# Kernel tuning notes

Measured on AMD Instinct MI355X. Metric: run time of the kernel, lower is better.

Reference implementation:

```python
import jax, jax.numpy as jnp
import numpy as np

U = 3072; I = 3072; N = U + I
D = 128; H = 4; HD = D // H
K = 10; BLOCKS = 2; RAW = 1280; DFF = 4 * D


def _pe_table(n, d):
    # standard sinusoidal positional encoding table [n, d]
    pos = jnp.arange(n, dtype=jnp.float32)[:, None]
    div = jnp.exp(jnp.arange(0, d, 2, dtype=jnp.float32) * (-np.log(10000.0) / d))
    ang = pos * div[None, :]
    pe = jnp.zeros((n, d), jnp.float32)
    return pe.at[:, 0::2].set(jnp.sin(ang)).at[:, 1::2].set(jnp.cos(ang))


def _ln(x, g, b, eps=1e-5):
    m = jnp.mean(x, -1, keepdims=True)
    v = jnp.var(x, -1, keepdims=True)
    return (x - m) * jax.lax.rsqrt(v + eps) * g + b


def _encoder(x, aw, ab, w1, b1, w2, b2, lng, lnb):
    # post-LN transformer encoder layer over sequence of all nodes of one type
    S = x.shape[0]
    q = (x @ aw[0] + ab[0]).reshape(S, H, HD)
    k = (x @ aw[1] + ab[1]).reshape(S, H, HD)
    v = (x @ aw[2] + ab[2]).reshape(S, H, HD)
    attn = jax.nn.softmax(jnp.einsum('shd,thd->hst', q, k) / np.sqrt(HD), axis=-1)
    o = jnp.einsum('hst,thd->shd', attn, v).reshape(S, D) @ aw[3] + ab[3]
    x = _ln(x + o, lng[0], lnb[0])
    f = jax.nn.relu(x @ w1 + b1) @ w2 + b2
    return _ln(x + f, lng[1], lnb[1])


def _topk_adj(emb, adj):
    # AttentionSampling(alpha=0.5, top_k=K): blend embedding similarity with adj,
    # keep adjacency entries at the per-row top-K positions (no_grad in original).
    e = jax.lax.stop_gradient(emb)
    score = 0.5 * (e @ e.T) + 0.5 * jax.lax.stop_gradient(adj)
    _, idx = jax.lax.top_k(score, K)  # [N, K]
    mask = jnp.zeros(adj.shape, adj.dtype).at[jnp.arange(adj.shape[0])[:, None], idx].set(1.0)
    return jax.lax.stop_gradient(mask) * adj


def _forward(adj, raw_nodes, proj_w, proj_b, user_emb, item_emb, visual_sim,
             alpha, pe_gate_w, pe_gate_b,
             u_attn_w, u_attn_b, u_ffn_w1, u_ffn_b1, u_ffn_w2, u_ffn_b2, u_ln_g, u_ln_b,
             i_attn_w, i_attn_b, i_ffn_w1, i_ffn_b1, i_ffn_w2, i_ffn_b2, i_ln_g, i_ln_b):
    eps = 1e-7
    # symmetric normalization of the item visual similarity matrix
    deg = jnp.sum(visual_sim, axis=1)
    dinv = jnp.power(deg + eps, -0.5)
    sim_norm = dinv[:, None] * visual_sim * dinv[None, :]
    pe = _pe_table(N, D)

    raw = raw_nodes @ proj_w + proj_b                       # [N, D]
    learned = jnp.concatenate([user_emb, item_emb], axis=0)  # [N, D]
    x = alpha * raw + (1.0 - alpha) * learned

    embeds_list = [x]
    for _ in range(BLOCKS):
        prev = embeds_list[-1]
        adj_topk = _topk_adj(prev, adj)
        # gnn_message_passing: spmm + visual similarity propagation on items
        cur = adj_topk @ prev
        cur = cur.at[U:].add(alpha * (sim_norm @ prev[U:]))
        # gated positional encoding on sampled nodes (all rows have top-K edges)
        gate = jax.nn.sigmoid(cur @ pe_gate_w + pe_gate_b)
        cur = cur + gate * pe
        u = _encoder(cur[:U], u_attn_w, u_attn_b, u_ffn_w1, u_ffn_b1,
                     u_ffn_w2, u_ffn_b2, u_ln_g, u_ln_b)
        it = _encoder(cur[U:], i_attn_w, i_attn_b, i_ffn_w1, i_ffn_b1,
                      i_ffn_w2, i_ffn_b2, i_ln_g, i_ln_b)
        embeds_list.append(jnp.concatenate([u, it], axis=0))

    w = jnp.linspace(1.0, 0.5, len(embeds_list))
    final = sum(wi * e for wi, e in zip(list(w), embeds_list))
    return final


def setup_inputs() -> dict:
    key = jax.random.key(0)
    ks = jax.random.split(key, 24)
    s = lambda i, shape, sc=0.05: jax.random.normal(ks[i], shape, jnp.float32) * sc
    u = jax.random.uniform(ks[20], (N, N), jnp.float32)
    adj = jnp.where(u < 0.005, 1.0, 0.0).astype(jnp.float32)  # sparse-pattern adjacency
    vs = jax.random.uniform(ks[21], (I, I), jnp.float32)
    visual_sim = (vs + vs.T) * 0.5
    return dict(
        adj=adj,
        raw_nodes=s(0, (N, RAW), 1.0),
        proj_w=s(1, (RAW, D)), proj_b=jnp.zeros((D,), jnp.float32),
        user_emb=s(2, (U, D), 0.1), item_emb=s(3, (I, D), 0.1),
        visual_sim=visual_sim,
        alpha=jnp.float32(0.5),
        pe_gate_w=s(4, (D, D), 0.01), pe_gate_b=jnp.full((D,), 0.5, jnp.float32),
        u_attn_w=s(5, (4, D, D)), u_attn_b=jnp.zeros((4, D), jnp.float32),
        u_ffn_w1=s(6, (D, DFF)), u_ffn_b1=jnp.zeros((DFF,), jnp.float32),
        u_ffn_w2=s(7, (DFF, D)), u_ffn_b2=jnp.zeros((D,), jnp.float32),
        u_ln_g=jnp.ones((2, D), jnp.float32), u_ln_b=jnp.zeros((2, D), jnp.float32),
        i_attn_w=s(8, (4, D, D)), i_attn_b=jnp.zeros((4, D), jnp.float32),
        i_ffn_w1=s(9, (D, DFF)), i_ffn_b1=jnp.zeros((DFF,), jnp.float32),
        i_ffn_w2=s(10, (DFF, D)), i_ffn_b2=jnp.zeros((D,), jnp.float32),
        i_ln_g=jnp.ones((2, D), jnp.float32), i_ln_b=jnp.zeros((2, D), jnp.float32),
    )


def reference(adj, raw_nodes, proj_w, proj_b, user_emb, item_emb, visual_sim, alpha,
              pe_gate_w, pe_gate_b,
              u_attn_w, u_attn_b, u_ffn_w1, u_ffn_b1, u_ffn_w2, u_ffn_b2, u_ln_g, u_ln_b,
              i_attn_w, i_attn_b, i_ffn_w1, i_ffn_b1, i_ffn_w2, i_ffn_b2, i_ln_g, i_ln_b):
    final = _forward(adj, raw_nodes, proj_w, proj_b, user_emb, item_emb, visual_sim,
                     alpha, pe_gate_w, pe_gate_b,
                     u_attn_w, u_attn_b, u_ffn_w1, u_ffn_b1, u_ffn_w2, u_ffn_b2, u_ln_g, u_ln_b,
                     i_attn_w, i_attn_b, i_ffn_w1, i_ffn_b1, i_ffn_w2, i_ffn_b2, i_ln_g, i_ln_b)
    return final, final[:U], final[U:]
```

## Files before the change

### kernel.cpp

```cpp
#include <hip/hip_runtime.h>
#include <math.h>

#define NTOT 6144
#define UU   3072
#define II   3072
#define DD   128
#define SS   3072
#define DFF2 512
#define HH   4

__global__ void pe_k(float* __restrict__ pe) {
  int idx = blockIdx.x * 256 + threadIdx.x;
  if (idx >= NTOT * 64) return;
  int pos = idx >> 6, j = idx & 63;
  float ex = (2.0f * (float)j) * (-0.07195578415606394f);
  float dv = expf(ex);
  float ang = (float)pos * dv;
  pe[(size_t)pos * DD + 2 * j]     = sinf(ang);
  pe[(size_t)pos * DD + 2 * j + 1] = cosf(ang);
}

__global__ void dinv_k(const float* __restrict__ vs, float* __restrict__ dinv) {
  int i = blockIdx.x, tid = threadIdx.x;
  __shared__ float red[256];
  float s = 0.f;
  const float* row = vs + (size_t)i * II;
  for (int j = tid; j < II; j += 256) s += row[j];
  red[tid] = s; __syncthreads();
  for (int st = 128; st > 0; st >>= 1) { if (tid < st) red[tid] += red[tid + st]; __syncthreads(); }
  if (tid == 0) dinv[i] = 1.0f / sqrtf(red[0] + 1e-7f);
}

__device__ __forceinline__ void gemm_core(
    const float* __restrict__ A, const float* __restrict__ B,
    int N, int K, int bm, int bn, int k0beg, int k0end,
    float (*As)[68], float (*Bs)[68], float (&acc)[4][4]) {
  const int tid = threadIdx.x;
  const int am = tid >> 2, ak = (tid & 3) * 4;
  const int bk = tid >> 4, bnc = (tid & 15) * 4;
  const float* Ap = A + (size_t)(bm + am) * K + ak;
  const float* Bp = B + (size_t)bk * N + bn + bnc;
  float4 av = *(const float4*)(Ap + k0beg);
  float4 bv = *(const float4*)(Bp + (size_t)k0beg * N);
  const int tx = tid & 15, ty = tid >> 4;
  for (int k0 = k0beg; k0 < k0end; k0 += 16) {
    __syncthreads();
    As[ak + 0][am] = av.x; As[ak + 1][am] = av.y;
    As[ak + 2][am] = av.z; As[ak + 3][am] = av.w;
    *(float4*)&Bs[bk][bnc] = bv;
    __syncthreads();
    if (k0 + 16 < k0end) {
      av = *(const float4*)(Ap + k0 + 16);
      bv = *(const float4*)(Bp + (size_t)(k0 + 16) * N);
    }
#pragma unroll
    for (int kq = 0; kq < 16; ++kq) {
      float4 a4 = *(const float4*)&As[kq][ty * 4];
      float4 b4 = *(const float4*)&Bs[kq][tx * 4];
      const float* ap = (const float*)&a4;
      const float* bp = (const float*)&b4;
#pragma unroll
      for (int i = 0; i < 4; ++i)
#pragma unroll
        for (int j = 0; j < 4; ++j)
          acc[i][j] = fmaf(ap[i], bp[j], acc[i][j]);
    }
  }
}

template<bool RELU>
__global__ __launch_bounds__(256, 4) void gemm_k(
    const float* __restrict__ A, const float* __restrict__ B,
    const float* __restrict__ bias, float* __restrict__ C,
    int M, int N, int K) {
  __shared__ float As[16][68];
  __shared__ float Bs[16][68];
  const int bm = blockIdx.y * 64, bn = blockIdx.x * 64;
  float acc[4][4] = {{0.f}};
  gemm_core(A, B, N, K, bm, bn, 0, K, As, Bs, acc);
  const int tx = threadIdx.x & 15, ty = threadIdx.x >> 4;
#pragma unroll
  for (int i = 0; i < 4; ++i) {
    int row = bm + ty * 4 + i;
    float4 o; float* op = (float*)&o;
#pragma unroll
    for (int j = 0; j < 4; ++j) {
      float v = acc[i][j] + (bias ? bias[bn + tx * 4 + j] : 0.0f);
      if (RELU) v = fmaxf(v, 0.0f);
      op[j] = v;
    }
    *(float4*)&C[(size_t)row * N + bn + tx * 4] = o;
  }
}

template<bool RELU>
__global__ __launch_bounds__(256, 4) void gemm2_k(
    const float* __restrict__ A, const float* __restrict__ Bu,
    const float* __restrict__ Bi, const float* __restrict__ biasu,
    const float* __restrict__ biasi, float* __restrict__ C,
    int N, int K) {
  __shared__ float As[16][68];
  __shared__ float Bs[16][68];
  const int bm = blockIdx.y * 64, bn = blockIdx.x * 64;
  const float* B    = (bm < UU) ? Bu : Bi;
  const float* bias = (bm < UU) ? biasu : biasi;
  float acc[4][4] = {{0.f}};
  gemm_core(A, B, N, K, bm, bn, 0, K, As, Bs, acc);
  const int tx = threadIdx.x & 15, ty = threadIdx.x >> 4;
#pragma unroll
  for (int i = 0; i < 4; ++i) {
    int row = bm + ty * 4 + i;
    float4 o; float* op = (float*)&o;
#pragma unroll
    for (int j = 0; j < 4; ++j) {
      float v = acc[i][j] + bias[bn + tx * 4 + j];
      if (RELU) v = fmaxf(v, 0.0f);
      op[j] = v;
    }
    *(float4*)&C[(size_t)row * N + bn + tx * 4] = o;
  }
}

__global__ __launch_bounds__(256, 4) void gemm_qkv2_k(
    const float* __restrict__ A, const float* __restrict__ Wu,
    const float* __restrict__ Wi, const float* __restrict__ Bu,
    const float* __restrict__ Bi, float* __restrict__ Cb) {
  __shared__ float As[16][68];
  __shared__ float Bs[16][68];
  const int mat = blockIdx.x >> 1;
  const int bn = (blockIdx.x & 1) * 64;
  const int bm = blockIdx.y * 64;
  const float* W    = ((bm < UU) ? Wu : Wi) + (size_t)mat * DD * DD;
  const float* bias = ((bm < UU) ? Bu : Bi) + mat * DD;
  float* C = Cb + (size_t)mat * NTOT * DD;
  float acc[4][4] = {{0.f}};
  gemm_core(A, W, DD, DD, bm, bn, 0, DD, As, Bs, acc);
  const int tx = threadIdx.x & 15, ty = threadIdx.x >> 4;
#pragma unroll
  for (int i = 0; i < 4; ++i) {
    int row = bm + ty * 4 + i;
    float4 o; float* op = (float*)&o;
#pragma unroll
    for (int j = 0; j < 4; ++j) op[j] = acc[i][j] + bias[bn + tx * 4 + j];
    *(float4*)&C[(size_t)row * DD + bn + tx * 4] = o;
  }
}

__global__ __launch_bounds__(256, 4) void gemm_blend_k(
    const float* __restrict__ A, const float* __restrict__ B,
    const float* __restrict__ bias, const float* __restrict__ ue,
    const float* __restrict__ ie, const float* __restrict__ alpha_p,
    float* __restrict__ C, int K) {
  __shared__ float As[16][68];
  __shared__ float Bs[16][68];
  const int bm = blockIdx.y * 64, bn = blockIdx.x * 64;
  float acc[4][4] = {{0.f}};
  gemm_core(A, B, DD, K, bm, bn, 0, K, As, Bs, acc);
  const int tx = threadIdx.x & 15, ty = threadIdx.x >> 4;
  float a = alpha_p[0];
#pragma unroll
  for (int i = 0; i < 4; ++i) {
    int row = bm + ty * 4 + i;
    const float* lrn = (row < UU) ? &ue[(size_t)row * DD]
                                  : &ie[(size_t)(row - UU) * DD];
    float4 lv = *(const float4*)&lrn[bn + tx * 4];
    const float* lp = (const float*)&lv;
    float4 o; float* op = (float*)&o;
#pragma unroll
    for (int j = 0; j < 4; ++j)
      op[j] = a * (acc[i][j] + bias[bn + tx * 4 + j]) + (1.0f - a) * lp[j];
    *(float4*)&C[(size_t)row * DD + bn + tx * 4] = o;
  }
}

__global__ __launch_bounds__(256, 4) void gemm_gate_k(
    const float* __restrict__ Acur, const float* __restrict__ B,
    const float* __restrict__ bias, const float* __restrict__ pe,
    float* __restrict__ Cout) {
  __shared__ float As[16][68];
  __shared__ float Bs[16][68];
  const int bm = blockIdx.y * 64, bn = blockIdx.x * 64;
  float acc[4][4] = {{0.f}};
  gemm_core(Acur, B, DD, DD, bm, bn, 0, DD, As, Bs, acc);
  const int tx = threadIdx.x & 15, ty = threadIdx.x >> 4;
#pragma unroll
  for (int i = 0; i < 4; ++i) {
    int row = bm + ty * 4 + i;
    float4 cv = *(const float4*)&Acur[(size_t)row * DD + bn + tx * 4];
    float4 pv = *(const float4*)&pe[(size_t)row * DD + bn + tx * 4];
    const float* cp = (const float*)&cv;
    const float* pp = (const float*)&pv;
    float4 o; float* op = (float*)&o;
#pragma unroll
    for (int j = 0; j < 4; ++j) {
      float v = acc[i][j] + bias[bn + tx * 4 + j];
      float g = 1.0f / (1.0f + expf(-v));
      op[j] = cp[j] + g * pp[j];
    }
    *(float4*)&Cout[(size_t)row * DD + bn + tx * 4] = o;
  }
}

__global__ __launch_bounds__(256, 4) void gemm_sk_k(
    const float* __restrict__ A, const float* __restrict__ B,
    const float* __restrict__ dinv, const float* __restrict__ alpha_p,
    float* __restrict__ C, int KCH) {
  __shared__ float As[16][68];
  __shared__ float Bs[16][68];
  const int N = DD, K = II;
  const int tid = threadIdx.x;
  const int am = tid >> 2, ak = (tid & 3) * 4;
  const int bk = tid >> 4, bnc = (tid & 15) * 4;
  const int bm = blockIdx.y * 64, bn = blockIdx.x * 64;
  const int kb = blockIdx.z * KCH, ke = kb + KCH;
  const float* Ap = A + (size_t)(bm + am) * K + ak;
  const float* Bp = B + (size_t)bk * N + bn + bnc;
  float4 av = *(const float4*)(Ap + kb);
  float4 bv = *(const float4*)(Bp + (size_t)kb * N);
  const int tx = tid & 15, ty = tid >> 4;
  float acc[4][4] = {{0.f}};
  for (int k0 = kb; k0 < ke; k0 += 16) {
    float ds = dinv[k0 + bk];
    __syncthreads();
    As[ak + 0][am] = av.x; As[ak + 1][am] = av.y;
    As[ak + 2][am] = av.z; As[ak + 3][am] = av.w;
    float4 sb = bv;
    sb.x *= ds; sb.y *= ds; sb.z *= ds; sb.w *= ds;
    *(float4*)&Bs[bk][bnc] = sb;
    __syncthreads();
    if (k0 + 16 < ke) {
      av = *(const float4*)(Ap + k0 + 16);
      bv = *(const float4*)(Bp + (size_t)(k0 + 16) * N);
    }
#pragma unroll
    for (int kq = 0; kq < 16; ++kq) {
      float4 a4 = *(const float4*)&As[kq][ty * 4];
      float4 b4 = *(const float4*)&Bs[kq][tx * 4];
      const float* ap = (const float*)&a4;
      const float* bp = (const float*)&b4;
#pragma unroll
      for (int i = 0; i < 4; ++i)
#pragma unroll
        for (int j = 0; j < 4; ++j)
          acc[i][j] = fmaf(ap[i], bp[j], acc[i][j]);
    }
  }
  float sc = alpha_p[0];
#pragma unroll
  for (int i = 0; i < 4; ++i) {
    int row = bm + ty * 4 + i;
    float rs = dinv[row] * sc;
#pragma unroll
    for (int j = 0; j < 4; ++j)
      atomicAdd(&C[(size_t)row * N + bn + tx * 4 + j], acc[i][j] * rs);
  }
}

__device__ __forceinline__ void ins10(float (&v)[10], int (&ix)[10], float cv, int ci) {
  if (!((cv > v[9]) || (cv == v[9] && ci < ix[9]))) return;
#pragma unroll
  for (int q = 0; q < 10; ++q) {
    bool b = (cv > v[q]) || (cv == v[q] && ci < ix[q]);
    float ov = v[q]; int oi = ix[q];
    if (b) { v[q] = cv; ix[q] = ci; cv = ov; ci = oi; }
  }
}

__global__ __launch_bounds__(256, 3) void topk_part_k(
    const float* __restrict__ E, const float* __restrict__ adj,
    float* __restrict__ topv, int* __restrict__ topi) {
  const int quarter = blockIdx.x;
  const int i0 = blockIdx.y * 32;
  const int jb = quarter * 1536;
  const int tid = threadIdx.x;
  const int a0 = tid & 15;
  const int b0 = tid >> 4;

  __shared__ __align__(16) unsigned char sm[50688];
  float4* Ei4 = (float4*)sm;
  float4* Ej4 = (float4*)(sm + 16896);
  float* dv   = (float*)(sm + 0);
  int*   di   = (int*)  (sm + 20736);
  float* redv = (float*)(sm + 41472);
  int*   redi = (int*)  (sm + 43648);
  float* wlv  = (float*)(sm + 45824);
  int*   wli  = (int*)  (sm + 47104);

  for (int p = 0; p < 4; ++p) {
    int l = tid + p * 256, r = l >> 5, c = l & 31;
    Ei4[r * 33 + c] = ((const float4*)(E + (size_t)(i0 + r) * DD))[c];
  }

  float v0[10], v1[10]; int y0[10], y1[10];
#pragma unroll
  for (int q = 0; q < 10; ++q) { v0[q] = -INFINITY; v1[q] = -INFINITY; y0[q] = 0x7fffffff; y1[q] = 0x7fffffff; }

  const float* arow0 = adj + (size_t)(i0 + a0) * NTOT;
  const float* arow1 = adj + (size_t)(i0 + a0 + 16) * NTOT;

  for (int jt = 0; jt < 24; ++jt) {
    const int jc = jb + jt * 64;
    __syncthreads();
#pragma unroll
    for (int p = 0; p < 8; ++p) {
      int l = tid + p * 256, r = l >> 5, c = l & 31;
      Ej4[r * 33 + c] = ((const float4*)(E + (size_t)(jc + r) * DD))[c];
    }
    __syncthreads();
    float ad0[4], ad1[4];
#pragma unroll
    for (int u = 0; u < 4; ++u) {
      int jg = jc + b0 + 16 * u;
      ad0[u] = arow0[jg];
      ad1[u] = arow1[jg];
    }
    float d0[4] = {0.f, 0.f, 0.f, 0.f}, d1[4] = {0.f, 0.f, 0.f, 0.f};
#pragma unroll 8
    for (int kq = 0; kq < 32; ++kq) {
      float4 aa = Ei4[a0 * 33 + kq];
      float4 ab = Ei4[(a0 + 16) * 33 + kq];
#pragma unroll
      for (int u = 0; u < 4; ++u) {
        float4 b = Ej4[(b0 + 16 * u) * 33 + kq];
        d0[u] = fmaf(aa.x, b.x, fmaf(aa.y, b.y, fmaf(aa.z, b.z, fmaf(aa.w, b.w, d0[u]))));
        d1[u] = fmaf(ab.x, b.x, fmaf(ab.y, b.y, fmaf(ab.z, b.z, fmaf(ab.w, b.w, d1[u]))));
      }
    }
#pragma unroll
    for (int u = 0; u < 4; ++u) {
      int jg = jc + b0 + 16 * u;
      ins10(v0, y0, 0.5f * d0[u] + 0.5f * ad0[u], jg);
      ins10(v1, y1, 0.5f * d1[u] + 0.5f * ad1[u], jg);
    }
  }

  __syncthreads();
  const int r0 = a0, r1 = a0 + 16;
#pragma unroll
  for (int q = 0; q < 10; ++q) {
    dv[r0 * 162 + b0 * 10 + q] = v0[q];  di[r0 * 162 + b0 * 10 + q] = y0[q];
    dv[r1 * 162 + b0 * 10 + q] = v1[q];  di[r1 * 162 + b0 * 10 + q] = y1[q];
  }
  __syncthreads();

  int p0 = 0, p1 = 0;
  for (int round = 0; round < 10; ++round) {
    float h0 = dv[r0 * 162 + b0 * 10 + p0]; int h0i = di[r0 * 162 + b0 * 10 + p0];
    float h1 = dv[r1 * 162 + b0 * 10 + p1]; int h1i = di[r1 * 162 + b0 * 10 + p1];
    redv[r0 * 17 + b0] = h0; redi[r0 * 17 + b0] = h0i;
    redv[r1 * 17 + b0] = h1; redi[r1 * 17 + b0] = h1i;
    __syncthreads();
    for (int st = 8; st >= 1; st >>= 1) {
      if (b0 < st) {
        float ov = redv[r0 * 17 + b0 + st]; int oi = redi[r0 * 17 + b0 + st];
        if (ov > redv[r0 * 17 + b0] || (ov == redv[r0 * 17 + b0] && oi < redi[r0 * 17 + b0])) {
          redv[r0 * 17 + b0] = ov; redi[r0 * 17 + b0] = oi;
        }
        ov = redv[r1 * 17 + b0 + st]; oi = redi[r1 * 17 + b0 + st];
        if (ov > redv[r1 * 17 + b0] || (ov == redv[r1 * 17 + b0] && oi < redi[r1 * 17 + b0])) {
          redv[r1 * 17 + b0] = ov; redi[r1 * 17 + b0] = oi;
        }
      }
      __syncthreads();
    }
    int w0 = redi[r0 * 17], w1 = redi[r1 * 17];
    if (b0 == 0) {
      wlv[r0 * 10 + round] = redv[r0 * 17]; wli[r0 * 10 + round] = w0;
      wlv[r1 * 10 + round] = redv[r1 * 17]; wli[r1 * 10 + round] = w1;
    }
    if (w0 == h0i) ++p0;
    if (w1 == h1i) ++p1;
    __syncthreads();
  }

  for (int t = tid; t < 320; t += 256) {
    int row = t / 10, q = t - row * 10;
    int gi = i0 + row;
    topv[(size_t)gi * 40 + quarter * 10 + q] = wlv[row * 10 + q];
    topi[(size_t)gi * 40 + quarter * 10 + q] = wli[row * 10 + q];
  }
}

__global__ __launch_bounds__(256) void topk_merge_k(
    const float* __restrict__ topv, const int* __restrict__ topi,
    const float* __restrict__ adj, const float* __restrict__ E,
    float* __restrict__ cur) {
  const int i0 = blockIdx.x * 16, tid = threadIdx.x;
  __shared__ int   midx[16][10];
  __shared__ float madj[16][10];
  if (tid < 16) {
    int row = i0 + tid;
    const float* va = topv + (size_t)row * 40;
    const int*   ia = topi + (size_t)row * 40;
    int pp0 = 0, pp1 = 0, pp2 = 0, pp3 = 0;
    for (int q = 0; q < 10; ++q) {
      float bv = va[pp0]; int bi = ia[pp0]; int bq = 0;
      float cv = va[10 + pp1]; int ci = ia[10 + pp1];
      if (cv > bv || (cv == bv && ci < bi)) { bv = cv; bi = ci; bq = 1; }
      cv = va[20 + pp2]; ci = ia[20 + pp2];
      if (cv > bv || (cv == bv && ci < bi)) { bv = cv; bi = ci; bq = 2; }
      cv = va[30 + pp3]; ci = ia[30 + pp3];
      if (cv > bv || (cv == bv && ci < bi)) { bv = cv; bi = ci; bq = 3; }
      if (bq == 0) ++pp0; else if (bq == 1) ++pp1; else if (bq == 2) ++pp2; else ++pp3;
      midx[tid][q] = bi;
      madj[tid][q] = adj[(size_t)row * NTOT + bi];
    }
  }
  __syncthreads();
  int d = tid & 127, hf = tid >> 7;
  for (int rr = 0; rr < 8; ++rr) {
    int r = rr * 2 + hf;
    float acc = 0.f;
#pragma unroll
    for (int w2 = 0; w2 < 10; ++w2) acc += madj[r][w2] * E[(size_t)midx[r][w2] * DD + d];
    cur[(size_t)(i0 + r) * DD + d] = acc;
  }
}

__global__ void final_k(const float* __restrict__ x0, const float* __restrict__ x1,
                        const float* __restrict__ x2, float* __restrict__ out) {
  int idx = blockIdx.x * 256 + threadIdx.x;
  if (idx >= NTOT * DD) return;
  float v = x0[idx] + 0.75f * x1[idx] + 0.5f * x2[idx];
  out[idx] = v;
  out[NTOT * DD + idx] = v;
}

__global__ __launch_bounds__(256, 3) void attn_k(
    const float* __restrict__ qkv, float* __restrict__ O) {
  const int qb = blockIdx.x * 16;
  const int hoff = blockIdx.y * 32;
  const int koff = (qb >= UU) ? UU : 0;
  const float* Q  = qkv;
  const float* Km = qkv + (size_t)NTOT * DD + (size_t)koff * DD;
  const float* V  = qkv + (size_t)2 * NTOT * DD + (size_t)koff * DD;
  const int tid = threadIdx.x;
  const int r = tid >> 4, g = tid & 15;
  const int jh = g >> 3, d4 = g & 7;
  __shared__ float4 Kt[64 * 9];
  __shared__ float4 Vt[64 * 9];
  __shared__ float  P[16 * 68];

  float4 qr[8];
  const float4* Qp = (const float4*)(Q + (size_t)(qb + r) * DD + hoff);
#pragma unroll
  for (int t = 0; t < 8; ++t) {
    float4 v = Qp[t];
    v.x *= 0.17677669529663687f; v.y *= 0.17677669529663687f;
    v.z *= 0.17677669529663687f; v.w *= 0.17677669529663687f;
    qr[t] = v;
  }
  float m_run = -INFINITY, l_run = 0.f;
  float4 acc = {0.f, 0.f, 0.f, 0.f};

  for (int t0 = 0; t0 < SS; t0 += 64) {
    __syncthreads();
#pragma unroll
    for (int p = 0; p < 2; ++p) {
      int l = tid + p * 256, row = l >> 3, c = l & 7;
      Kt[row * 9 + c] = ((const float4*)(Km + (size_t)(t0 + row) * DD + hoff))[c];
      Vt[row * 9 + c] = ((const float4*)(V  + (size_t)(t0 + row) * DD + hoff))[c];
    }
    __syncthreads();
    float s[4];
#pragma unroll
    for (int q = 0; q < 4; ++q) {
      const float4* Kr = &Kt[(g + 16 * q) * 9];
      float d = 0.f;
#pragma unroll
      for (int t = 0; t < 8; ++t) {
        float4 a = qr[t], b = Kr[t];
        d = fmaf(a.x, b.x, fmaf(a.y, b.y, fmaf(a.z, b.z, fmaf(a.w, b.w, d))));
      }
      s[q] = d;
    }
    float tm = fmaxf(fmaxf(s[0], s[1]), fmaxf(s[2], s[3]));
#pragma unroll
    for (int off = 1; off < 16; off <<= 1) tm = fmaxf(tm, __shfl_xor(tm, off, 64));
    float m_new = fmaxf(m_run, tm);
    float sc = expf(m_run - m_new);
    float ts = 0.f;
#pragma unroll
    for (int q = 0; q < 4; ++q) {
      float p = expf(s[q] - m_new);
      ts += p;
      P[r * 68 + g + 16 * q] = p;
    }
#pragma unroll
    for (int off = 1; off < 16; off <<= 1) ts += __shfl_xor(ts, off, 64);
    l_run = l_run * sc + ts;
    m_run = m_new;
    acc.x *= sc; acc.y *= sc; acc.z *= sc; acc.w *= sc;
    __syncthreads();
    const float* Prow = &P[r * 68 + jh * 32];
#pragma unroll
    for (int jj4 = 0; jj4 < 8; ++jj4) {
      float4 pv = *(const float4*)(Prow + jj4 * 4);
      const float* pp = (const float*)&pv;
#pragma unroll
      for (int c = 0; c < 4; ++c) {
        float4 v4 = Vt[(jh * 32 + jj4 * 4 + c) * 9 + d4];
        acc.x = fmaf(pp[c], v4.x, acc.x);
        acc.y = fmaf(pp[c], v4.y, acc.y);
        acc.z = fmaf(pp[c], v4.z, acc.z);
        acc.w = fmaf(pp[c], v4.w, acc.w);
      }
    }
  }
  acc.x += __shfl_xor(acc.x, 8, 64);
  acc.y += __shfl_xor(acc.y, 8, 64);
  acc.z += __shfl_xor(acc.z, 8, 64);
  acc.w += __shfl_xor(acc.w, 8, 64);
  if (jh == 0) {
    float inv = 1.0f / l_run;
    float4 o = {acc.x * inv, acc.y * inv, acc.z * inv, acc.w * inv};
    *(float4*)(O + (size_t)(qb + r) * DD + hoff + d4 * 4) = o;
  }
}

__global__ void add_ln2_k(const float* __restrict__ X, const float* __restrict__ Y,
                          const float* __restrict__ gu, const float* __restrict__ bu,
                          const float* __restrict__ gi, const float* __restrict__ bi,
                          float* __restrict__ Out) {
  int row = blockIdx.x, tid = threadIdx.x;
  const float* g = (row < UU) ? gu : gi;
  const float* b = (row < UU) ? bu : bi;
  __shared__ float red[128];
  float v = X[(size_t)row * DD + tid] + Y[(size_t)row * DD + tid];
  red[tid] = v; __syncthreads();
  for (int st = 64; st > 0; st >>= 1) { if (tid < st) red[tid] += red[tid + st]; __syncthreads(); }
  float mean = red[0] * (1.0f / DD); __syncthreads();
  float d = v - mean;
  red[tid] = d * d; __syncthreads();
  for (int st = 64; st > 0; st >>= 1) { if (tid < st) red[tid] += red[tid + st]; __syncthreads(); }
  float var = red[0] * (1.0f / DD); __syncthreads();
  Out[(size_t)row * DD + tid] = d * (1.0f / sqrtf(var + 1e-5f)) * g[tid] + b[tid];
}

extern "C" void kernel_launch(void* const* d_in, const int* in_sizes, int n_in,
                              void* d_out, int out_size, void* d_ws, size_t ws_size,
                              hipStream_t stream) {
  (void)in_sizes; (void)n_in; (void)out_size; (void)ws_size;
  const float* adj       = (const float*)d_in[0];
  const float* raw_nodes = (const float*)d_in[1];
  const float* proj_w    = (const float*)d_in[2];
  const float* proj_b    = (const float*)d_in[3];
  const float* user_emb  = (const float*)d_in[4];
  const float* item_emb  = (const float*)d_in[5];
  const float* vs        = (const float*)d_in[6];
  const float* alpha_p   = (const float*)d_in[7];
  const float* pgw       = (const float*)d_in[8];
  const float* pgb       = (const float*)d_in[9];
  const float* uaw = (const float*)d_in[10];
  const float* uab = (const float*)d_in[11];
  const float* uw1 = (const float*)d_in[12];
  const float* ub1 = (const float*)d_in[13];
  const float* uw2 = (const float*)d_in[14];
  const float* ub2 = (const float*)d_in[15];
  const float* ulg = (const float*)d_in[16];
  const float* ulb = (const float*)d_in[17];
  const float* iaw = (const float*)d_in[18];
  const float* iab = (const float*)d_in[19];
  const float* iw1 = (const float*)d_in[20];
  const float* ib1 = (const float*)d_in[21];
  const float* iw2 = (const float*)d_in[22];
  const float* ib2 = (const float*)d_in[23];
  const float* ilg = (const float*)d_in[24];
  const float* ilb = (const float*)d_in[25];

  float* w = (float*)d_ws;
  float* pe   = w; w += (size_t)NTOT * DD;
  float* x0   = w; w += (size_t)NTOT * DD;
  float* x1   = w; w += (size_t)NTOT * DD;
  float* x2   = w; w += (size_t)NTOT * DD;
  float* cur  = w; w += (size_t)NTOT * DD;
  float* curg = w; w += (size_t)NTOT * DD;
  float* qkv  = w; w += (size_t)3 * NTOT * DD;
  float* xl   = w; w += (size_t)NTOT * DD;
  float* f2   = w; w += (size_t)NTOT * DD;
  float* t1   = w; w += (size_t)NTOT * DFF2;
  float* dinv = w; w += 4096;
  float* ao   = t1;
  float* topv = qkv;
  int*   topi = (int*)(qkv + (size_t)NTOT * DD);

  pe_k<<<(NTOT * 64 + 255) / 256, 256, 0, stream>>>(pe);
  dinv_k<<<II, 256, 0, stream>>>(vs, dinv);
  gemm_blend_k<<<dim3(2, NTOT / 64), 256, 0, stream>>>(
      raw_nodes, proj_w, proj_b, user_emb, item_emb, alpha_p, x0, 1280);

  float* xs[3] = {x0, x1, x2};
  for (int b = 0; b < 2; ++b) {
    const float* prev = xs[b];
    float* outb = xs[b + 1];
    topk_part_k<<<dim3(4, 192), 256, 0, stream>>>(prev, adj, topv, topi);
    topk_merge_k<<<NTOT / 16, 256, 0, stream>>>(topv, topi, adj, prev, cur);
    gemm_sk_k<<<dim3(2, II / 64, 4), 256, 0, stream>>>(
        vs, prev + (size_t)UU * DD, dinv, alpha_p, cur + (size_t)UU * DD, 768);
    gemm_gate_k<<<dim3(2, NTOT / 64), 256, 0, stream>>>(cur, pgw, pgb, pe, curg);
    gemm_qkv2_k<<<dim3(6, NTOT / 64), 256, 0, stream>>>(curg, uaw, iaw, uab, iab, qkv);
    attn_k<<<dim3(NTOT / 16, HH), 256, 0, stream>>>(qkv, ao);
    gemm2_k<false><<<dim3(2, NTOT / 64), 256, 0, stream>>>(
        ao, uaw + 3 * DD * DD, iaw + 3 * DD * DD, uab + 3 * DD, iab + 3 * DD, f2, DD, DD);
    add_ln2_k<<<NTOT, 128, 0, stream>>>(curg, f2, ulg, ulb, ilg, ilb, xl);
    gemm2_k<true ><<<dim3(8, NTOT / 64), 256, 0, stream>>>(
        xl, uw1, iw1, ub1, ib1, t1, DFF2, DD);
    gemm2_k<false><<<dim3(2, NTOT / 64), 256, 0, stream>>>(
        t1, uw2, iw2, ub2, ib2, f2, DD, DFF2);
    add_ln2_k<<<NTOT, 128, 0, stream>>>(xl, f2, ulg + DD, ulb + DD, ilg + DD, ilb + DD, outb);
  }
  final_k<<<(NTOT * DD + 255) / 256, 256, 0, stream>>>(x0, x1, x2, (float*)d_out);
}
```

Baseline: 1.963 ms.

## Retile top-k similarity kernel with packed 64-bit keys and widen attention query tiles

The top-k partial kernel now processes 64 rows by 128 columns per tile over eighths of the columns, with 4x8 register blocking. Each score and its index are packed into one 64-bit key so insertion is a single compare, and the 16 per-thread lists are merged with wave shuffles instead of shared-memory reduction rounds. The merge kernel combines eight partial lists. The attention kernel now handles 32 query rows per block, two per thread, so each K/V tile loaded into shared memory is reused twice. This adds register pressure: occupancy drops to 2 blocks per SM for topk, and attn keeps more accumulators live.

After: 1.830 ms. 1.07x faster.

```diff
diff --git a/kernel.cpp b/kernel.cpp
--- a/kernel.cpp
+++ b/kernel.cpp
@@ -256,133 +256,125 @@
   }
 }
 
-__device__ __forceinline__ void ins10(float (&v)[10], int (&ix)[10], float cv, int ci) {
-  if (!((cv > v[9]) || (cv == v[9] && ci < ix[9]))) return;
+__device__ __forceinline__ unsigned long long packsc(float v, int idx) {
+  unsigned int b = __float_as_uint(v);
+  b ^= (b & 0x80000000u) ? 0xFFFFFFFFu : 0x80000000u;
+  return ((unsigned long long)b << 32) | (unsigned int)(0xFFFFFFFFu ^ (unsigned int)idx);
+}
+
+__device__ __forceinline__ void ins10u(unsigned long long (&v)[10], unsigned long long c) {
+  if (c <= v[9]) return;
 #pragma unroll
   for (int q = 0; q < 10; ++q) {
-    bool b = (cv > v[q]) || (cv == v[q] && ci < ix[q]);
-    float ov = v[q]; int oi = ix[q];
-    if (b) { v[q] = cv; ix[q] = ci; cv = ov; ci = oi; }
-  }
-}
-
-__global__ __launch_bounds__(256, 3) void topk_part_k(
+    unsigned long long ov = v[q];
+    if (c > ov) { v[q] = c; c = ov; }
+  }
+}
+
+__device__ __forceinline__ unsigned long long shflx_u64(unsigned long long v, int off) {
+  unsigned int lo = (unsigned int)v, hi = (unsigned int)(v >> 32);
+  lo = __shfl_xor(lo, off, 64);
+  hi = __shfl_xor(hi, off, 64);
+  return ((unsigned long long)hi << 32) | lo;
+}
+
+__global__ __launch_bounds__(256, 2) void topk_part_k(
     const float* __restrict__ E, const float* __restrict__ adj,
-    float* __restrict__ topv, int* __restrict__ topi) {
-  const int quarter = blockIdx.x;
-  const int i0 = blockIdx.y * 32;
-  const int jb = quarter * 1536;
+    unsigned long long* __restrict__ top8) {
+  const int eighth = blockIdx.x;
+  const int i0 = blockIdx.y * 64;
+  const int jb = eighth * 768;
   const int tid = threadIdx.x;
-  const int a0 = tid & 15;
-  const int b0 = tid >> 4;
-
-  __shared__ __align__(16) unsigned char sm[50688];
-  float4* Ei4 = (float4*)sm;
-  float4* Ej4 = (float4*)(sm + 16896);
-  float* dv   = (float*)(sm + 0);
-  int*   di   = (int*)  (sm + 20736);
-  float* redv = (float*)(sm + 41472);
-  int*   redi = (int*)  (sm + 43648);
-  float* wlv  = (float*)(sm + 45824);
-  int*   wli  = (int*)  (sm + 47104);
-
-  for (int p = 0; p < 4; ++p) {
-    int l = tid + p * 256, r = l >> 5, c = l & 31;
-    Ei4[r * 33 + c] = ((const float4*)(E + (size_t)(i0 + r) * DD))[c];
-  }
-
-  float v0[10], v1[10]; int y0[10], y1[10];
-#pragma unroll
-  for (int q = 0; q < 10; ++q) { v0[q] = -INFINITY; v1[q] = -INFINITY; y0[q] = 0x7fffffff; y1[q] = 0x7fffffff; }
-
-  const float* arow0 = adj + (size_t)(i0 + a0) * NTOT;
-  const float* arow1 = adj + (size_t)(i0 + a0 + 16) * NTOT;
-
-  for (int jt = 0; jt < 24; ++jt) {
-    const int jc = jb + jt * 64;
-    __syncthreads();
-#pragma unroll
-    for (int p = 0; p < 8; ++p) {
-      int l = tid + p * 256, r = l >> 5, c = l & 31;
-      Ej4[r * 33 + c] = ((const float4*)(E + (size_t)(jc + r) * DD))[c];
-    }
-    __syncthreads();
-    float ad0[4], ad1[4];
-#pragma unroll
-    for (int u = 0; u < 4; ++u) {
-      int jg = jc + b0 + 16 * u;
-      ad0[u] = arow0[jg];
-      ad1[u] = arow1[jg];
-    }
-    float d0[4] = {0.f, 0.f, 0.f, 0.f}, d1[4] = {0.f, 0.f, 0.f, 0.f};
-#pragma unroll 8
-    for (int kq = 0; kq < 32; ++kq) {
-      float4 aa = Ei4[a0 * 33 + kq];
-      float4 ab = Ei4[(a0 + 16) * 33 + kq];
-#pragma unroll
-      for (int u = 0; u < 4; ++u) {
-        float4 b = Ej4[(b0 + 16 * u) * 33 + kq];
-        d0[u] = fmaf(aa.x, b.x, fmaf(aa.y, b.y, fmaf(aa.z, b.z, fmaf(aa.w, b.w, d0[u]))));
-        d1[u] = fmaf(ab.x, b.x, fmaf(ab.y, b.y, fmaf(ab.z, b.z, fmaf(ab.w, b.w, d1[u]))));
-      }
-    }
-#pragma unroll
-    for (int u = 0; u < 4; ++u) {
-      int jg = jc + b0 + 16 * u;
-      ins10(v0, y0, 0.5f * d0[u] + 0.5f * ad0[u], jg);
-      ins10(v1, y1, 0.5f * d1[u] + 0.5f * ad1[u], jg);
-    }
-  }
-
-  __syncthreads();
-  const int r0 = a0, r1 = a0 + 16;
-#pragma unroll
-  for (int q = 0; q < 10; ++q) {
-    dv[r0 * 162 + b0 * 10 + q] = v0[q];  di[r0 * 162 + b0 * 10 + q] = y0[q];
-    dv[r1 * 162 + b0 * 10 + q] = v1[q];  di[r1 * 162 + b0 * 10 + q] = y1[q];
-  }
-  __syncthreads();
-
-  int p0 = 0, p1 = 0;
-  for (int round = 0; round < 10; ++round) {
-    float h0 = dv[r0 * 162 + b0 * 10 + p0]; int h0i = di[r0 * 162 + b0 * 10 + p0];
-    float h1 = dv[r1 * 162 + b0 * 10 + p1]; int h1i = di[r1 * 162 + b0 * 10 + p1];
-    redv[r0 * 17 + b0] = h0; redi[r0 * 17 + b0] = h0i;
-    redv[r1 * 17 + b0] = h1; redi[r1 * 17 + b0] = h1i;
-    __syncthreads();
-    for (int st = 8; st >= 1; st >>= 1) {
-      if (b0 < st) {
-        float ov = redv[r0 * 17 + b0 + st]; int oi = redi[r0 * 17 + b0 + st];
-        if (ov > redv[r0 * 17 + b0] || (ov == redv[r0 * 17 + b0] && oi < redi[r0 * 17 + b0])) {
-          redv[r0 * 17 + b0] = ov; redi[r0 * 17 + b0] = oi;
+  const int a = tid >> 4;
+  const int b = tid & 15;
+
+  __shared__ float4 Eis[64 * 17];
+  __shared__ float4 Ejs[128 * 17];
+  const float4* E4 = (const float4*)E;
+
+  unsigned long long lst[4][10];
+#pragma unroll
+  for (int m = 0; m < 4; ++m)
+#pragma unroll
+    for (int q = 0; q < 10; ++q) lst[m][q] = 0ULL;
+
+  for (int jt = 0; jt < 6; ++jt) {
+    const int jc = jb + jt * 128;
+    float acc[4][8];
+#pragma unroll
+    for (int m = 0; m < 4; ++m)
+#pragma unroll
+      for (int u = 0; u < 8; ++u) acc[m][u] = 0.f;
+
+    for (int kh = 0; kh < 2; ++kh) {
+      __syncthreads();
+#pragma unroll
+      for (int p = 0; p < 4; ++p) {
+        int l = tid + p * 256, row = l >> 4, c = l & 15;
+        Eis[row * 17 + c] = E4[(size_t)(i0 + row) * 32 + kh * 16 + c];
+      }
+#pragma unroll
+      for (int p = 0; p < 8; ++p) {
+        int l = tid + p * 256, row = l >> 4, c = l & 15;
+        Ejs[row * 17 + c] = E4[(size_t)(jc + row) * 32 + kh * 16 + c];
+      }
+      __syncthreads();
+#pragma unroll 4
+      for (int kq = 0; kq < 16; ++kq) {
+        float4 a0 = Eis[a * 17 + kq];
+        float4 a1 = Eis[(a + 16) * 17 + kq];
+        float4 a2 = Eis[(a + 32) * 17 + kq];
+        float4 a3 = Eis[(a + 48) * 17 + kq];
+#pragma unroll
+        for (int u = 0; u < 8; ++u) {
+          float4 bf = Ejs[(b + 16 * u) * 17 + kq];
+          acc[0][u] = fmaf(a0.x, bf.x, fmaf(a0.y, bf.y, fmaf(a0.z, bf.z, fmaf(a0.w, bf.w, acc[0][u]))));
+          acc[1][u] = fmaf(a1.x, bf.x, fmaf(a1.y, bf.y, fmaf(a1.z, bf.z, fmaf(a1.w, bf.w, acc[1][u]))));
+          acc[2][u] = fmaf(a2.x, bf.x, fmaf(a2.y, bf.y, fmaf(a2.z, bf.z, fmaf(a2.w, bf.w, acc[2][u]))));
+          acc[3][u] = fmaf(a3.x, bf.x, fmaf(a3.y, bf.y, fmaf(a3.z, bf.z, fmaf(a3.w, bf.w, acc[3][u]))));
         }
-        ov = redv[r1 * 17 + b0 + st]; oi = redi[r1 * 17 + b0 + st];
-        if (ov > redv[r1 * 17 + b0] || (ov == redv[r1 * 17 + b0] && oi < redi[r1 * 17 + b0])) {
-          redv[r1 * 17 + b0] = ov; redi[r1 * 17 + b0] = oi;
-        }
-      }
-      __syncthreads();
-    }
-    int w0 = redi[r0 * 17], w1 = redi[r1 * 17];
-    if (b0 == 0) {
-      wlv[r0 * 10 + round] = redv[r0 * 17]; wli[r0 * 10 + round] = w0;
-      wlv[r1 * 10 + round] = redv[r1 * 17]; wli[r1 * 10 + round] = w1;
-    }
-    if (w0 == h0i) ++p0;
-    if (w1 == h1i) ++p1;
-    __syncthreads();
-  }
-
-  for (int t = tid; t < 320; t += 256) {
-    int row = t / 10, q = t - row * 10;
-    int gi = i0 + row;
-    topv[(size_t)gi * 40 + quarter * 10 + q] = wlv[row * 10 + q];
-    topi[(size_t)gi * 40 + quarter * 10 + q] = wli[row * 10 + q];
+      }
+    }
+#pragma unroll
+    for (int m = 0; m < 4; ++m) {
+      const float* ar = adj + (size_t)(i0 + a + 16 * m) * NTOT + jc + b;
+#pragma unroll
+      for (int u = 0; u < 8; ++u) {
+        float sc = 0.5f * acc[m][u] + 0.5f * ar[16 * u];
+        ins10u(lst[m], packsc(sc, jc + b + 16 * u));
+      }
+    }
+  }
+
+#pragma unroll
+  for (int m = 0; m < 4; ++m) {
+    unsigned long long ow[10];
+#pragma unroll
+    for (int round = 0; round < 10; ++round) {
+      unsigned long long h = lst[m][0];
+      unsigned long long w = h;
+#pragma unroll
+      for (int off = 1; off < 16; off <<= 1) {
+        unsigned long long o = shflx_u64(w, off);
+        if (o > w) w = o;
+      }
+      ow[round] = w;
+      if (h == w) {
+#pragma unroll
+        for (int q = 0; q < 9; ++q) lst[m][q] = lst[m][q + 1];
+      }
+    }
+    if (b == 0) {
+      int grow = i0 + a + 16 * m;
+#pragma unroll
+      for (int q = 0; q < 10; ++q)
+        top8[(size_t)grow * 80 + eighth * 10 + q] = ow[q];
+    }
   }
 }
 
 __global__ __launch_bounds__(256) void topk_merge_k(
-    const float* __restrict__ topv, const int* __restrict__ topi,
+    const unsigned long long* __restrict__ top8,
     const float* __restrict__ adj, const float* __restrict__ E,
     float* __restrict__ cur) {
   const int i0 = blockIdx.x * 16, tid = threadIdx.x;
@@ -390,20 +382,20 @@
   __shared__ float madj[16][10];
   if (tid < 16) {
     int row = i0 + tid;
-    const float* va = topv + (size_t)row * 40;
-    const int*   ia = topi + (size_t)row * 40;
-    int pp0 = 0, pp1 = 0, pp2 = 0, pp3 = 0;
+    const unsigned long long* L = top8 + (size_t)row * 80;
+    int p[8] = {0, 0, 0, 0, 0, 0, 0, 0};
     for (int q = 0; q < 10; ++q) {
-      float bv = va[pp0]; int bi = ia[pp0]; int bq = 0;
-      float cv = va[10 + pp1]; int ci = ia[10 + pp1];
-      if (cv > bv || (cv == bv && ci < bi)) { bv = cv; bi = ci; bq = 1; }
-      cv = va[20 + pp2]; ci = ia[20 + pp2];
-      if (cv > bv || (cv == bv && ci < bi)) { bv = cv; bi = ci; bq = 2; }
-      cv = va[30 + pp3]; ci = ia[30 + pp3];
-      if (cv > bv || (cv == bv && ci < bi)) { bv = cv; bi = ci; bq = 3; }
-      if (bq == 0) ++pp0; else if (bq == 1) ++pp1; else if (bq == 2) ++pp2; else ++pp3;
-      midx[tid][q] = bi;
-      madj[tid][q] = adj[(size_t)row * NTOT + bi];
+      unsigned long long best = 0ULL; int be = 0;
+#pragma unroll
+      for (int e = 0; e < 8; ++e) {
+        unsigned long long h = (p[e] < 10) ? L[e * 10 + p[e]] : 0ULL;
+        if (h > best) { best = h; be = e; }
+      }
+#pragma unroll
+      for (int e = 0; e < 8; ++e) p[e] += (e == be) ? 1 : 0;
+      int idx = (int)(0xFFFFFFFFu ^ (unsigned int)best);
+      midx[tid][q] = idx;
+      madj[tid][q] = adj[(size_t)row * NTOT + idx];
     }
   }
   __syncthreads();
@@ -428,7 +420,7 @@
 
 __global__ __launch_bounds__(256, 3) void attn_k(
     const float* __restrict__ qkv, float* __restrict__ O) {
-  const int qb = blockIdx.x * 16;
+  const int qb = blockIdx.x * 32;
   const int hoff = blockIdx.y * 32;
   const int koff = (qb >= UU) ? UU : 0;
   const float* Q  = qkv;
@@ -439,19 +431,24 @@
   const int jh = g >> 3, d4 = g & 7;
   __shared__ float4 Kt[64 * 9];
   __shared__ float4 Vt[64 * 9];
-  __shared__ float  P[16 * 68];
-
-  float4 qr[8];
-  const float4* Qp = (const float4*)(Q + (size_t)(qb + r) * DD + hoff);
+  __shared__ float  P[32 * 68];
+
+  float4 q0[8], q1[8];
+  const float4* Qp0 = (const float4*)(Q + (size_t)(qb + r) * DD + hoff);
+  const float4* Qp1 = (const float4*)(Q + (size_t)(qb + r + 16) * DD + hoff);
 #pragma unroll
   for (int t = 0; t < 8; ++t) {
-    float4 v = Qp[t];
+    float4 v = Qp0[t];
     v.x *= 0.17677669529663687f; v.y *= 0.17677669529663687f;
     v.z *= 0.17677669529663687f; v.w *= 0.17677669529663687f;
-    qr[t] = v;
-  }
-  float m_run = -INFINITY, l_run = 0.f;
-  float4 acc = {0.f, 0.f, 0.f, 0.f};
+    q0[t] = v;
+    v = Qp1[t];
+    v.x *= 0.17677669529663687f; v.y *= 0.17677669529663687f;
+    v.z *= 0.17677669529663687f; v.w *= 0.17677669529663687f;
+    q1[t] = v;
+  }
+  float m0 = -INFINITY, l0 = 0.f, m1 = -INFINITY, l1 = 0.f;
+  float4 acc0 = {0.f, 0.f, 0.f, 0.f}, acc1 = {0.f, 0.f, 0.f, 0.f};
 
   for (int t0 = 0; t0 < SS; t0 += 64) {
     __syncthreads();
@@ -462,59 +459,83 @@
       Vt[row * 9 + c] = ((const float4*)(V  + (size_t)(t0 + row) * DD + hoff))[c];
     }
     __syncthreads();
-    float s[4];
-#pragma unroll
-    for (int q = 0; q < 4; ++q) {
-      const float4* Kr = &Kt[(g + 16 * q) * 9];
-      float d = 0.f;
+    float s0[4], s1[4];
+#pragma unroll
+    for (int u = 0; u < 4; ++u) {
+      const float4* Kr = &Kt[(g + 16 * u) * 9];
+      float d0 = 0.f, d1 = 0.f;
 #pragma unroll
       for (int t = 0; t < 8; ++t) {
-        float4 a = qr[t], b = Kr[t];
-        d = fmaf(a.x, b.x, fmaf(a.y, b.y, fmaf(a.z, b.z, fmaf(a.w, b.w, d))));
-      }
-      s[q] = d;
-    }
-    float tm = fmaxf(fmaxf(s[0], s[1]), fmaxf(s[2], s[3]));
-#pragma unroll
-    for (int off = 1; off < 16; off <<= 1) tm = fmaxf(tm, __shfl_xor(tm, off, 64));
-    float m_new = fmaxf(m_run, tm);
-    float sc = expf(m_run - m_new);
-    float ts = 0.f;
-#pragma unroll
-    for (int q = 0; q < 4; ++q) {
-      float p = expf(s[q] - m_new);
-      ts += p;
-      P[r * 68 + g + 16 * q] = p;
-    }
-#pragma unroll
-    for (int off = 1; off < 16; off <<= 1) ts += __shfl_xor(ts, off, 64);
-    l_run = l_run * sc + ts;
-    m_run = m_new;
-    acc.x *= sc; acc.y *= sc; acc.z *= sc; acc.w *= sc;
+        float4 kb = Kr[t];
+        float4 a0 = q0[t], a1 = q1[t];
+        d0 = fmaf(a0.x, kb.x, fmaf(a0.y, kb.y, fmaf(a0.z, kb.z, fmaf(a0.w, kb.w, d0))));
+        d1 = fmaf(a1.x, kb.x, fmaf(a1.y, kb.y, fmaf(a1.z, kb.z, fmaf(a1.w, kb.w, d1))));
+      }
+      s0[u] = d0; s1[u] = d1;
+    }
+    float tm0 = fmaxf(fmaxf(s0[0], s0[1]), fmaxf(s0[2], s0[3]));
+    float tm1 = fmaxf(fmaxf(s1[0], s1[1]), fmaxf(s1[2], s1[3]));
+#pragma unroll
+    for (int off = 1; off < 16; off <<= 1) {
+      tm0 = fmaxf(tm0, __shfl_xor(tm0, off, 64));
+      tm1 = fmaxf(tm1, __shfl_xor(tm1, off, 64));
+    }
+    float n0 = fmaxf(m0, tm0), n1 = fmaxf(m1, tm1);
+    float sc0 = expf(m0 - n0), sc1 = expf(m1 - n1);
+    float ts0 = 0.f, ts1 = 0.f;
+#pragma unroll
+    for (int u = 0; u < 4; ++u) {
+      float p0 = expf(s0[u] - n0), p1 = expf(s1[u] - n1);
+      ts0 += p0; ts1 += p1;
+      P[r * 68 + g + 16 * u] = p0;
+      P[(r + 16) * 68 + g + 16 * u] = p1;
+    }
+#pragma unroll
+    for (int off = 1; off < 16; off <<= 1) {
+      ts0 += __shfl_xor(ts0, off, 64);
+      ts1 += __shfl_xor(ts1, off, 64);
+    }
+    l0 = l0 * sc0 + ts0; m0 = n0;
+    l1 = l1 * sc1 + ts1; m1 = n1;
+    acc0.x *= sc0; acc0.y *= sc0; acc0.z *= sc0; acc0.w *= sc0;
+    acc1.x *= sc1; acc1.y *= sc1; acc1.z *= sc1; acc1.w *= sc1;
     __syncthreads();
-    const float* Prow = &P[r * 68 + jh * 32];
+    const float* Pr0 = &P[r * 68 + jh * 32];
+    const float* Pr1 = &P[(r + 16) * 68 + jh * 32];
 #pragma unroll
     for (int jj4 = 0; jj4 < 8; ++jj4) {
-      float4 pv = *(const float4*)(Prow + jj4 * 4);
-      const float* pp = (const float*)&pv;
+      float4 pv0 = *(const float4*)(Pr0 + jj4 * 4);
+      float4 pv1 = *(const float4*)(Pr1 + jj4 * 4);
+      const float* pp0 = (const float*)&pv0;
+      const float* pp1 = (const float*)&pv1;
 #pragma unroll
       for (int c = 0; c < 4; ++c) {
         float4 v4 = Vt[(jh * 32 + jj4 * 4 + c) * 9 + d4];
-        acc.x = fmaf(pp[c], v4.x, acc.x);
-        acc.y = fmaf(pp[c], v4.y, acc.y);
-        acc.z = fmaf(pp[c], v4.z, acc.z);
-        acc.w = fmaf(pp[c], v4.w, acc.w);
-      }
-    }
-  }
-  acc.x += __shfl_xor(acc.x, 8, 64);
-  acc.y += __shfl_xor(acc.y, 8, 64);
-  acc.z += __shfl_xor(acc.z, 8, 64);
-  acc.w += __shfl_xor(acc.w, 8, 64);
+        acc0.x = fmaf(pp0[c], v4.x, acc0.x);
+        acc0.y = fmaf(pp0[c], v4.y, acc0.y);
+        acc0.z = fmaf(pp0[c], v4.z, acc0.z);
+        acc0.w = fmaf(pp0[c], v4.w, acc0.w);
+        acc1.x = fmaf(pp1[c], v4.x, acc1.x);
+        acc1.y = fmaf(pp1[c], v4.y, acc1.y);
+        acc1.z = fmaf(pp1[c], v4.z, acc1.z);
+        acc1.w = fmaf(pp1[c], v4.w, acc1.w);
+      }
+    }
+  }
+  acc0.x += __shfl_xor(acc0.x, 8, 64);
+  acc0.y += __shfl_xor(acc0.y, 8, 64);
+  acc0.z += __shfl_xor(acc0.z, 8, 64);
+  acc0.w += __shfl_xor(acc0.w, 8, 64);
+  acc1.x += __shfl_xor(acc1.x, 8, 64);
+  acc1.y += __shfl_xor(acc1.y, 8, 64);
+  acc1.z += __shfl_xor(acc1.z, 8, 64);
+  acc1.w += __shfl_xor(acc1.w, 8, 64);
   if (jh == 0) {
-    float inv = 1.0f / l_run;
-    float4 o = {acc.x * inv, acc.y * inv, acc.z * inv, acc.w * inv};
-    *(float4*)(O + (size_t)(qb + r) * DD + hoff + d4 * 4) = o;
+    float i0v = 1.0f / l0, i1v = 1.0f / l1;
+    float4 o0 = {acc0.x * i0v, acc0.y * i0v, acc0.z * i0v, acc0.w * i0v};
+    float4 o1 = {acc1.x * i1v, acc1.y * i1v, acc1.z * i1v, acc1.w * i1v};
+    *(float4*)(O + (size_t)(qb + r) * DD + hoff + d4 * 4) = o0;
+    *(float4*)(O + (size_t)(qb + r + 16) * DD + hoff + d4 * 4) = o1;
   }
 }
 
@@ -581,8 +602,7 @@
   float* t1   = w; w += (size_t)NTOT * DFF2;
   float* dinv = w; w += 4096;
   float* ao   = t1;
-  float* topv = qkv;
-  int*   topi = (int*)(qkv + (size_t)NTOT * DD);
+  unsigned long long* top8 = (unsigned long long*)qkv;
 
   pe_k<<<(NTOT * 64 + 255) / 256, 256, 0, stream>>>(pe);
   dinv_k<<<II, 256, 0, stream>>>(vs, dinv);
@@ -593,13 +613,13 @@
   for (int b = 0; b < 2; ++b) {
     const float* prev = xs[b];
     float* outb = xs[b + 1];
-    topk_part_k<<<dim3(4, 192), 256, 0, stream>>>(prev, adj, topv, topi);
-    topk_merge_k<<<NTOT / 16, 256, 0, stream>>>(topv, topi, adj, prev, cur);
+    topk_part_k<<<dim3(8, 96), 256, 0, stream>>>(prev, adj, top8);
+    topk_merge_k<<<NTOT / 16, 256, 0, stream>>>(top8, adj, prev, cur);
     gemm_sk_k<<<dim3(2, II / 64, 4), 256, 0, stream>>>(
         vs, prev + (size_t)UU * DD, dinv, alpha_p, cur + (size_t)UU * DD, 768);
     gemm_gate_k<<<dim3(2, NTOT / 64), 256, 0, stream>>>(cur, pgw, pgb, pe, curg);
     gemm_qkv2_k<<<dim3(6, NTOT / 64), 256, 0, stream>>>(curg, uaw, iaw, uab, iab, qkv);
-    attn_k<<<dim3(NTOT / 16, HH), 256, 0, stream>>>(qkv, ao);
+    attn_k<<<dim3(NTOT / 32, HH), 256, 0, stream>>>(qkv, ao);
     gemm2_k<false><<<dim3(2, NTOT / 64), 256, 0, stream>>>(
         ao, uaw + 3 * DD * DD, iaw + 3 * DD * DD, uab + 3 * DD, iab + 3 * DD, f2, DD, DD);
     add_ln2_k<<<NTOT, 128, 0, stream>>>(curg, f2, ulg, ulb, ilg, ilb, xl);
```
